# Kernel optimization log

Measured on AMD Instinct MI355X. Metric: run time of the kernel, lower is better.

## Reference

```python
import jax, jax.numpy as jnp
import numpy as np

# 4D conv over (L, P, W, H) decomposed as k shifted 3D convs over (P, W, H),
# with the L spatial dim folded into the batch. Faithful to convNd(num_dims=4),
# stride 1, 'same' padding (padding = (k-1)//2), no bias.

def conv4d(x, w):
    # x: [B, C, L, P, W, H]; w: [O, I, k, k, k, k]
    k = w.shape[2]
    p = (k - 1) // 2
    B, C, L, P, Wd, Hd = x.shape
    O = w.shape[0]
    xp = jnp.pad(x, ((0, 0), (0, 0), (p, p), (0, 0), (0, 0), (0, 0)))
    dn = ('NCDHW', 'OIDHW', 'NCDHW')
    out = jnp.zeros((B, O, L, P, Wd, Hd), x.dtype)
    for dl in range(k):  # k <= 3, static loop over kernel taps along L
        xs = xp[:, :, dl:dl + L]                                  # [B,C,L,P,W,H]
        xs = xs.transpose(0, 2, 1, 3, 4, 5).reshape(B * L, C, P, Wd, Hd)
        y = jax.lax.conv_general_dilated(xs, w[:, :, dl], (1, 1, 1),
                                         [(p, p)] * 3, dimension_numbers=dn)
        out = out + y.reshape(B, L, O, P, Wd, Hd).transpose(0, 2, 1, 3, 4, 5)
    return out


def inception4d(x, weights):
    # mean over parallel 4D convs with kernel sizes 1, 3, ... (2i+1)
    acc = conv4d(x, weights[0])
    for w in weights[1:]:
        acc = acc + conv4d(x, w)
    return acc / len(weights)


def setup_inputs() -> dict:
    key = jax.random.key(0)
    ks = jax.random.split(key, 5)
    B, T, W, H, C = 4, 48, 8, 8, 32
    d_model, d_ff = 32, 64
    x = jax.random.normal(ks[0], (B, T, W, H, C), dtype=jnp.float32)
    # Inception_Block4D weights: kernel sizes 1 and 3 (num_kernels=2), no bias
    w1_0 = jax.random.normal(ks[1], (d_ff, d_model, 1, 1, 1, 1), dtype=jnp.float32) * 0.1
    w1_1 = jax.random.normal(ks[2], (d_ff, d_model, 3, 3, 3, 3), dtype=jnp.float32) * 0.02
    w2_0 = jax.random.normal(ks[3], (d_model, d_ff, 1, 1, 1, 1), dtype=jnp.float32) * 0.1
    w2_1 = jax.random.normal(ks[4], (d_model, d_ff, 3, 3, 3, 3), dtype=jnp.float32) * 0.02
    return {"x": x, "w1_0": w1_0, "w1_1": w1_1, "w2_0": w2_0, "w2_1": w2_1}


def reference(x, w1_0, w1_1, w2_0, w2_1):
    B, T, W, H, C = x.shape
    periods = (2, 3, 4)                       # FFT_for_Period hardcoded output
    xf = jnp.ones((B, len(periods)), x.dtype) # hardcoded uniform weights
    real_len = T                              # seq_len + pred_len
    res = []
    for period in periods:
        if real_len % period != 0:
            length = (real_len // period + 1) * period
            out = jnp.concatenate([x, x[:, -(length - real_len):]], axis=1)
        else:
            length = real_len
            out = x
        # [B, L, P, W, H, C] -> [B, C, L, P, W, H]
        out = out.reshape(B, length // period, period, W, H, C).transpose(0, 5, 1, 2, 3, 4)
        h = inception4d(out, [w1_0, w1_1])
        h = jax.nn.gelu(h, approximate=False)  # torch nn.GELU default (exact)
        h = inception4d(h, [w2_0, w2_1])
        # [B, C, L, P, W, H] -> [B, (L P), W, H, C]
        h = h.transpose(0, 2, 3, 4, 5, 1).reshape(B, length, W, H, C)
        res.append(h[:, :real_len])
    res = jnp.stack(res, axis=1)              # [B, k, T, W, H, C]
    pw = jax.nn.softmax(xf, axis=1).reshape(B, len(periods), 1, 1, 1, 1)
    return jnp.sum(res * pw, axis=1) + x
```

## Files before the change

kernel.cpp:

```cpp
#include <hip/hip_runtime.h>
#include <math.h>


typedef __attribute__((ext_vector_type(8))) short bf16x8;
typedef __attribute__((ext_vector_type(4))) float f32x4;
typedef unsigned short u16;

#define XC 3200
#define HC2 7168
#define XSEG 617600
#define ZSEG_END 639104
#define W1OFF 639104
#define W2OFF 804992
#define H1OFF 970880
#define H1P 1383424
#define PREP_N 970880
#define OUT_Q 98304
#define PREP_TOT (PREP_N + OUT_Q)

#define WAITVM(N) asm volatile("s_waitcnt vmcnt(" #N ")" ::: "memory")
#define SBAR()    asm volatile("s_barrier" ::: "memory")

__device__ __forceinline__ u16 f2bf(float f) {
    unsigned u = __float_as_uint(f);
    unsigned r = u + 0x7fffu + ((u >> 16) & 1u);
    return (u16)(r >> 16);
}
__device__ __forceinline__ float gelu_exact(float v) {
    return 0.5f * v * (1.0f + erff(v * 0.7071067811865476f));
}

__device__ __forceinline__ void cp1k(const u16* g, u16* l, int lane) {
    __builtin_amdgcn_global_load_lds(
        (const __attribute__((address_space(1))) unsigned int*)(g + lane * 8),
        (__attribute__((address_space(3))) unsigned int*)(l + lane * 8),
        16, 0, 0);
}

__global__ __launch_bounds__(256) void prep(
    const float* __restrict__ x,
    const float* __restrict__ w1_0, const float* __restrict__ w1_1,
    const float* __restrict__ w2_0, const float* __restrict__ w2_1,
    u16* __restrict__ ws, float* __restrict__ out) {
    int i = blockIdx.x * 256 + threadIdx.x;
    if (i < XSEG) {
        int cellidx = i / XC; int inner = i - cellidx * XC;
        int cellpos = inner >> 5; int low = inner & 31;
        int sc = low >> 3, jj = low & 7;
        int c = ((sc ^ (cellpos & 3)) << 3) + jj;
        int wp = cellpos / 10, hp = cellpos - (cellpos / 10) * 10;
        float v = 0.f;
        if (cellidx < 192 && wp >= 1 && wp <= 8 && hp >= 1 && hp <= 8)
            v = x[(cellidx * 64 + (wp - 1) * 8 + (hp - 1)) * 32 + c];
        ws[i] = f2bf(v);
    } else if (i < ZSEG_END) {
        int j = i - XSEG;
        int per = j / 7168; int off = j - per * 7168;
        ws[H1OFF + per * H1P + 192 * 7168 + off] = 0;
    } else if (i < W2OFF) {
        int j = i - W1OFF;
        int tap = j >> 11; int r = j & 2047;
        int nh = r >> 10; int rr = r & 1023;
        int chunkh = rr >> 3, jj = rr & 7;
        int m = chunkh & 15, nq = (chunkh >> 4) & 1, quad = chunkh >> 5;
        int o = nh * 32 + nq * 16 + m, c = quad * 8 + jj;
        float v = 0.5f * w1_1[(o * 32 + c) * 81 + tap];
        if (tap == 40) v += 0.5f * w1_0[o * 32 + c];
        ws[i] = f2bf(v);
    } else if (i < PREP_N) {
        int j = i - W2OFF;
        int tap = j >> 11; int r = j & 2047;
        int kh = r >> 10; int rr = r & 1023;
        int chunkh = rr >> 3, jj = rr & 7;
        int m = chunkh & 15, nt = (chunkh >> 4) & 1, quad = chunkh >> 5;
        int o = nt * 16 + m, c = kh * 32 + quad * 8 + jj;
        float v = 0.5f * w2_1[(o * 64 + c) * 81 + tap];
        if (tap == 40) v += 0.5f * w2_0[o * 64 + c];
        ws[i] = f2bf(v);
    } else if (i < PREP_TOT) {
        int j = i - PREP_N;
        ((float4*)out)[j] = ((const float4*)x)[j];
    }
}

template<int P>
__device__ __forceinline__ void conv1_body(
    const u16* __restrict__ xs, const u16* __restrict__ w1b,
    u16* __restrict__ h1, int tpp, int bb, int nh,
    u16* __restrict__ s_a, u16* __restrict__ s_w) {
    constexpr int HB = (P == 2) ? 0 : (P == 3) ? H1P : 2 * H1P;
    constexpr int L = 48 / P;
    constexpr int EXT = P + 1;
    constexpr int NW = 6 + 2 * EXT;
    constexpr int ZS = NW;
    constexpr int NP = (NW + 1) * 7;

    int tid = threadIdx.x;
    int lane = tid & 63, wv = tid >> 6;
    int m = lane & 15, quad = lane >> 4;
    int ts = wv >> 1, mh = wv & 1;
    int t0 = tpp * 6, t = t0 + ts;
    int l = t / P, q = t - l * P;

    int sp[2];
#pragma unroll
    for (int mtl = 0; mtl < 2; ++mtl) {
        int pos = (mh * 2 + mtl) * 16 + m;
        sp[mtl] = (pos >> 3) * 10 + (pos & 7);
    }

    f32x4 acc[2][2];
#pragma unroll
    for (int mtl = 0; mtl < 2; ++mtl)
#pragma unroll
        for (int nq = 0; nq < 2; ++nq) acc[mtl][nq] = f32x4{0.f, 0.f, 0.f, 0.f};

    for (int p = wv; p < NP; p += 12) {
        int si = p / 7, pc = p - si * 7;
        int tt = t0 - EXT + si;
        int cell = (si == ZS) ? 192
                 : (((unsigned)tt < 48u) ? bb * 48 + tt : 192);
        cp1k(xs + cell * XC + pc * 512, s_a + si * 3584 + pc * 512, lane);
    }
    if (wv < 6) {
        cp1k(w1b + (0 * 3 + (wv >> 1)) * 2048 + nh * 1024 + (wv & 1) * 512,
             s_w + 0 * 3072 + wv * 512, lane);
        cp1k(w1b + (1 * 3 + (wv >> 1)) * 2048 + nh * 1024 + (wv & 1) * 512,
             s_w + 1 * 3072 + wv * 512, lane);
        WAITVM(1);
    } else {
        WAITVM(0);
    }
    SBAR();

#pragma unroll 1
    for (int cg = 0; cg < 27; ++cg) {
        if (wv < 6 && cg < 25)
            cp1k(w1b + ((cg + 2) * 3 + (wv >> 1)) * 2048 + nh * 1024 +
                     (wv & 1) * 512,
                 s_w + ((cg + 2) & 3) * 3072 + wv * 512, lane);
        if (cg < 25)       { WAITVM(2); }
        else if (cg == 25) { WAITVM(1); }
        else               { WAITVM(0); }
        SBAR();

        int g2 = cg / 3, dw = cg - g2 * 3;
        int dl = g2 / 3, dq = g2 - dl * 3;
        int lq = l + dl - 1, qq = q + dq - 1;
        bool valid = ((unsigned)lq < (unsigned)L) &&
                     ((unsigned)qq < (unsigned)P);
        int si = valid ? (ts + dl * P + dq) : ZS;
        const u16* ba = s_a + si * 3584;
        const u16* bw = s_w + (cg & 3) * 3072;
#pragma unroll
        for (int j = 0; j < 3; ++j) {
            const u16* tw = bw + j * 1024;
            bf16x8 wf0 = *(const bf16x8*)(tw + (((quad * 2 + 0) * 16 + m) << 3));
            bf16x8 wf1 = *(const bf16x8*)(tw + (((quad * 2 + 1) * 16 + m) << 3));
#pragma unroll
            for (int mtl = 0; mtl < 2; ++mtl) {
                int cellpos = sp[mtl] + dw * 10 + j;
                bf16x8 af = *(const bf16x8*)(ba + cellpos * 32 +
                                             ((quad ^ (cellpos & 3)) << 3));
                acc[mtl][0] = __builtin_amdgcn_mfma_f32_16x16x32_bf16(
                    af, wf0, acc[mtl][0], 0, 0, 0);
                acc[mtl][1] = __builtin_amdgcn_mfma_f32_16x16x32_bf16(
                    af, wf1, acc[mtl][1], 0, 0, 0);
            }
        }
    }

    u16* hh = h1 + HB + (bb * 48 + t) * HC2 + nh * 3584;
#pragma unroll
    for (int mtl = 0; mtl < 2; ++mtl)
#pragma unroll
        for (int r = 0; r < 4; ++r) {
            int pos = (mh * 2 + mtl) * 16 + quad * 4 + r;
            int cellpos = ((pos >> 3) + 1) * 10 + (pos & 7) + 1;
#pragma unroll
            for (int nq = 0; nq < 2; ++nq) {
                int ol = nq * 16 + m;
                hh[cellpos * 32 + (((ol >> 3) ^ (cellpos & 3)) << 3) + (ol & 7)] =
                    f2bf(gelu_exact(acc[mtl][nq][r]));
            }
        }
#pragma unroll
    for (int it = 0; it < 5; ++it) {
        int k = it * 768 + tid;
        if (k < 3456) {
            int tc = k / 576; int rr = k - tc * 576;
            int bp = rr >> 4, u = rr & 15;
            int cp;
            if (bp < 10) cp = bp;
            else if (bp < 20) cp = 90 + (bp - 10);
            else if (bp < 28) cp = (bp - 19) * 10;
            else cp = (bp - 27) * 10 + 9;
            unsigned int* h32 = (unsigned int*)(h1 + HB +
                (bb * 48 + t0 + tc) * HC2 + nh * 3584);
            h32[cp * 16 + u] = 0;
        }
    }
}

__global__ __launch_bounds__(768) void conv1_k(
    const u16* __restrict__ ws_x, const u16* __restrict__ ws_w1,
    u16* __restrict__ ws_h1) {
    __shared__ __align__(16) u16 s_a[17 * 3584];
    __shared__ __align__(16) u16 s_w[4 * 3072];
    int g = blockIdx.x;
    int jid = (g & 7) * 24 + (g >> 3);
    int per = jid / 64; int rem = jid - per * 64;
    int bb = rem / 16; int r2 = rem - bb * 16;
    int tpp = r2 >> 1, nh = r2 & 1;
    if (per == 0)      conv1_body<2>(ws_x, ws_w1, ws_h1, tpp, bb, nh, s_a, s_w);
    else if (per == 1) conv1_body<3>(ws_x, ws_w1, ws_h1, tpp, bb, nh, s_a, s_w);
    else               conv1_body<4>(ws_x, ws_w1, ws_h1, tpp, bb, nh, s_a, s_w);
}

template<int P>
__device__ __forceinline__ void conv2_body(
    const u16* __restrict__ h1, const u16* __restrict__ w2b,
    float* __restrict__ out, int tpp, int bb, int kh,
    u16* __restrict__ s_a, u16* __restrict__ s_w) {
    constexpr int HB = (P == 2) ? 0 : (P == 3) ? H1P : 2 * H1P;
    constexpr int L = 48 / P;
    constexpr int EXT = P + 1;
    constexpr int NW = 6 + 2 * EXT;
    constexpr int ZS = NW;
    constexpr int NP = (NW + 1) * 7;

    int tid = threadIdx.x;
    int lane = tid & 63, wv = tid >> 6;
    int m = lane & 15, quad = lane >> 4;
    int ts = wv >> 1, mh = wv & 1;
    int t0 = tpp * 6, t = t0 + ts;
    int l = t / P, q = t - l * P;
    const u16* hb = h1 + HB;

    int sp[2];
#pragma unroll
    for (int mtl = 0; mtl < 2; ++mtl) {
        int pos = (mh * 2 + mtl) * 16 + m;
        sp[mtl] = (pos >> 3) * 10 + (pos & 7);
    }

    f32x4 acc[2][2];
#pragma unroll
    for (int mtl = 0; mtl < 2; ++mtl)
#pragma unroll
        for (int nt = 0; nt < 2; ++nt) acc[mtl][nt] = f32x4{0.f, 0.f, 0.f, 0.f};

    for (int p = wv; p < NP; p += 12) {
        int si = p / 7, pc = p - si * 7;
        int tt = t0 - EXT + si;
        int cell = (si == ZS) ? 192
                 : (((unsigned)tt < 48u) ? bb * 48 + tt : 192);
        cp1k(hb + cell * HC2 + kh * 3584 + pc * 512,
             s_a + si * 3584 + pc * 512, lane);
    }
    if (wv < 6) {
        cp1k(w2b + (0 * 3 + (wv >> 1)) * 2048 + kh * 1024 + (wv & 1) * 512,
             s_w + 0 * 3072 + wv * 512, lane);
        cp1k(w2b + (1 * 3 + (wv >> 1)) * 2048 + kh * 1024 + (wv & 1) * 512,
             s_w + 1 * 3072 + wv * 512, lane);
        WAITVM(1);
    } else {
        WAITVM(0);
    }
    SBAR();

#pragma unroll 1
    for (int cg = 0; cg < 27; ++cg) {
        if (wv < 6 && cg < 25)
            cp1k(w2b + ((cg + 2) * 3 + (wv >> 1)) * 2048 + kh * 1024 +
                     (wv & 1) * 512,
                 s_w + ((cg + 2) & 3) * 3072 + wv * 512, lane);
        if (cg < 25)       { WAITVM(2); }
        else if (cg == 25) { WAITVM(1); }
        else               { WAITVM(0); }
        SBAR();

        int g2 = cg / 3, dw = cg - g2 * 3;
        int dl = g2 / 3, dq = g2 - dl * 3;
        int lq = l + dl - 1, qq = q + dq - 1;
        bool valid = ((unsigned)lq < (unsigned)L) &&
                     ((unsigned)qq < (unsigned)P);
        int si = valid ? (ts + dl * P + dq) : ZS;
        const u16* ba = s_a + si * 3584;
        const u16* bw = s_w + (cg & 3) * 3072;
#pragma unroll
        for (int j = 0; j < 3; ++j) {
            const u16* tw = bw + j * 1024;
            bf16x8 wf0 = *(const bf16x8*)(tw + (((quad * 2 + 0) * 16 + m) << 3));
            bf16x8 wf1 = *(const bf16x8*)(tw + (((quad * 2 + 1) * 16 + m) << 3));
#pragma unroll
            for (int mtl = 0; mtl < 2; ++mtl) {
                int cellpos = sp[mtl] + dw * 10 + j;
                bf16x8 af = *(const bf16x8*)(ba + cellpos * 32 +
                                             ((quad ^ (cellpos & 3)) << 3));
                acc[mtl][0] = __builtin_amdgcn_mfma_f32_16x16x32_bf16(
                    af, wf0, acc[mtl][0], 0, 0, 0);
                acc[mtl][1] = __builtin_amdgcn_mfma_f32_16x16x32_bf16(
                    af, wf1, acc[mtl][1], 0, 0, 0);
            }
        }
    }

    float* orow = out + (bb * 48 + t) * 2048;
    const float s = 1.0f / 3.0f;
#pragma unroll
    for (int mtl = 0; mtl < 2; ++mtl)
#pragma unroll
        for (int nt = 0; nt < 2; ++nt)
#pragma unroll
            for (int r = 0; r < 4; ++r) {
                int pos = (mh * 2 + mtl) * 16 + quad * 4 + r;
                atomicAdd(&orow[pos * 32 + nt * 16 + m], acc[mtl][nt][r] * s);
            }
}

__global__ __launch_bounds__(768) void conv2_k(
    const u16* __restrict__ ws_h1, const u16* __restrict__ ws_w2,
    float* __restrict__ out) {
    __shared__ __align__(16) u16 s_a[17 * 3584];
    __shared__ __align__(16) u16 s_w[4 * 3072];
    int g = blockIdx.x;
    int jid = (g & 7) * 24 + (g >> 3);
    int per = jid / 64; int rem = jid - per * 64;
    int bb = rem / 16; int r2 = rem - bb * 16;
    int tpp = r2 >> 1, kh = r2 & 1;
    if (per == 0)      conv2_body<2>(ws_h1, ws_w2, out, tpp, bb, kh, s_a, s_w);
    else if (per == 1) conv2_body<3>(ws_h1, ws_w2, out, tpp, bb, kh, s_a, s_w);
    else               conv2_body<4>(ws_h1, ws_w2, out, tpp, bb, kh, s_a, s_w);
}

extern "C" void kernel_launch(void* const* d_in, const int* in_sizes, int n_in,
                              void* d_out, int out_size, void* d_ws, size_t ws_size,
                              hipStream_t stream) {
    const float* x    = (const float*)d_in[0];
    const float* w1_0 = (const float*)d_in[1];
    const float* w1_1 = (const float*)d_in[2];
    const float* w2_0 = (const float*)d_in[3];
    const float* w2_1 = (const float*)d_in[4];
    float* out = (float*)d_out;

    u16* ws = (u16*)d_ws;
    u16* ws_x  = ws;
    u16* ws_w1 = ws + W1OFF;
    u16* ws_w2 = ws + W2OFF;
    u16* ws_h1 = ws + H1OFF;

    prep<<<(PREP_TOT + 255) / 256, 256, 0, stream>>>(
        x, w1_0, w1_1, w2_0, w2_1, ws, out);
    conv1_k<<<192, 768, 0, stream>>>(ws_x, ws_w1, ws_h1);
    conv2_k<<<192, 768, 0, stream>>>(ws_h1, ws_w2, out);
}
```

Baseline: 118.9 us.

## Stage weights per 9-tap group with double buffering, cutting barriers from 27 to 9

```diff
diff --git a/kernel.cpp b/kernel.cpp
--- a/kernel.cpp
+++ b/kernel.cpp
@@ -115,6 +115,17 @@
 #pragma unroll
         for (int nq = 0; nq < 2; ++nq) acc[mtl][nq] = f32x4{0.f, 0.f, 0.f, 0.f};
 
+    auto stageS = [&](int sg) {
+        const u16* src = w1b + nh * 1024;
+        u16* dst = s_w + (sg & 1) * 9216;
+#pragma unroll
+        for (int i = 0; i < 2; ++i) {
+            int k = wv * 2 + i; if (k >= 18) k = 17;
+            cp1k(src + (sg * 9 + (k >> 1)) * 2048 + (k & 1) * 512,
+                 dst + k * 512, lane);
+        }
+    };
+
     for (int p = wv; p < NP; p += 12) {
         int si = p / 7, pc = p - si * 7;
         int tt = t0 - EXT + si;
@@ -122,52 +133,41 @@
                  : (((unsigned)tt < 48u) ? bb * 48 + tt : 192);
         cp1k(xs + cell * XC + pc * 512, s_a + si * 3584 + pc * 512, lane);
     }
-    if (wv < 6) {
-        cp1k(w1b + (0 * 3 + (wv >> 1)) * 2048 + nh * 1024 + (wv & 1) * 512,
-             s_w + 0 * 3072 + wv * 512, lane);
-        cp1k(w1b + (1 * 3 + (wv >> 1)) * 2048 + nh * 1024 + (wv & 1) * 512,
-             s_w + 1 * 3072 + wv * 512, lane);
-        WAITVM(1);
-    } else {
-        WAITVM(0);
-    }
-    SBAR();
+    stageS(0);
+    WAITVM(0); SBAR();
 
 #pragma unroll 1
-    for (int cg = 0; cg < 27; ++cg) {
-        if (wv < 6 && cg < 25)
-            cp1k(w1b + ((cg + 2) * 3 + (wv >> 1)) * 2048 + nh * 1024 +
-                     (wv & 1) * 512,
-                 s_w + ((cg + 2) & 3) * 3072 + wv * 512, lane);
-        if (cg < 25)       { WAITVM(2); }
-        else if (cg == 25) { WAITVM(1); }
-        else               { WAITVM(0); }
-        SBAR();
-
-        int g2 = cg / 3, dw = cg - g2 * 3;
-        int dl = g2 / 3, dq = g2 - dl * 3;
+    for (int g = 0; g < 9; ++g) {
+        if (g < 8) stageS(g + 1);
+
+        int dl = g / 3, dq = g - dl * 3;
         int lq = l + dl - 1, qq = q + dq - 1;
         bool valid = ((unsigned)lq < (unsigned)L) &&
                      ((unsigned)qq < (unsigned)P);
         int si = valid ? (ts + dl * P + dq) : ZS;
         const u16* ba = s_a + si * 3584;
-        const u16* bw = s_w + (cg & 3) * 3072;
-#pragma unroll
-        for (int j = 0; j < 3; ++j) {
-            const u16* tw = bw + j * 1024;
-            bf16x8 wf0 = *(const bf16x8*)(tw + (((quad * 2 + 0) * 16 + m) << 3));
-            bf16x8 wf1 = *(const bf16x8*)(tw + (((quad * 2 + 1) * 16 + m) << 3));
-#pragma unroll
-            for (int mtl = 0; mtl < 2; ++mtl) {
-                int cellpos = sp[mtl] + dw * 10 + j;
-                bf16x8 af = *(const bf16x8*)(ba + cellpos * 32 +
-                                             ((quad ^ (cellpos & 3)) << 3));
-                acc[mtl][0] = __builtin_amdgcn_mfma_f32_16x16x32_bf16(
-                    af, wf0, acc[mtl][0], 0, 0, 0);
-                acc[mtl][1] = __builtin_amdgcn_mfma_f32_16x16x32_bf16(
-                    af, wf1, acc[mtl][1], 0, 0, 0);
+        const u16* bw = s_w + (g & 1) * 9216;
+#pragma unroll
+        for (int dw = 0; dw < 3; ++dw)
+#pragma unroll
+            for (int j = 0; j < 3; ++j) {
+                const u16* tw = bw + (dw * 3 + j) * 1024;
+                bf16x8 wf0 = *(const bf16x8*)(tw +
+                    (((quad * 2 + 0) * 16 + m) << 3));
+                bf16x8 wf1 = *(const bf16x8*)(tw +
+                    (((quad * 2 + 1) * 16 + m) << 3));
+#pragma unroll
+                for (int mtl = 0; mtl < 2; ++mtl) {
+                    int cellpos = sp[mtl] + dw * 10 + j;
+                    bf16x8 af = *(const bf16x8*)(ba + cellpos * 32 +
+                                                 ((quad ^ (cellpos & 3)) << 3));
+                    acc[mtl][0] = __builtin_amdgcn_mfma_f32_16x16x32_bf16(
+                        af, wf0, acc[mtl][0], 0, 0, 0);
+                    acc[mtl][1] = __builtin_amdgcn_mfma_f32_16x16x32_bf16(
+                        af, wf1, acc[mtl][1], 0, 0, 0);
+                }
             }
-        }
+        if (g < 8) { WAITVM(0); SBAR(); }
     }
 
     u16* hh = h1 + HB + (bb * 48 + t) * HC2 + nh * 3584;
@@ -206,7 +206,7 @@
     const u16* __restrict__ ws_x, const u16* __restrict__ ws_w1,
     u16* __restrict__ ws_h1) {
     __shared__ __align__(16) u16 s_a[17 * 3584];
-    __shared__ __align__(16) u16 s_w[4 * 3072];
+    __shared__ __align__(16) u16 s_w[2 * 9216];
     int g = blockIdx.x;
     int jid = (g & 7) * 24 + (g >> 3);
     int per = jid / 64; int rem = jid - per * 64;
@@ -250,6 +250,17 @@
 #pragma unroll
         for (int nt = 0; nt < 2; ++nt) acc[mtl][nt] = f32x4{0.f, 0.f, 0.f, 0.f};
 
+    auto stageS = [&](int sg) {
+        const u16* src = w2b + kh * 1024;
+        u16* dst = s_w + (sg & 1) * 9216;
+#pragma unroll
+        for (int i = 0; i < 2; ++i) {
+            int k = wv * 2 + i; if (k >= 18) k = 17;
+            cp1k(src + (sg * 9 + (k >> 1)) * 2048 + (k & 1) * 512,
+                 dst + k * 512, lane);
+        }
+    };
+
     for (int p = wv; p < NP; p += 12) {
         int si = p / 7, pc = p - si * 7;
         int tt = t0 - EXT + si;
@@ -258,52 +269,41 @@
         cp1k(hb + cell * HC2 + kh * 3584 + pc * 512,
              s_a + si * 3584 + pc * 512, lane);
     }
-    if (wv < 6) {
-        cp1k(w2b + (0 * 3 + (wv >> 1)) * 2048 + kh * 1024 + (wv & 1) * 512,
-             s_w + 0 * 3072 + wv * 512, lane);
-        cp1k(w2b + (1 * 3 + (wv >> 1)) * 2048 + kh * 1024 + (wv & 1) * 512,
-             s_w + 1 * 3072 + wv * 512, lane);
-        WAITVM(1);
-    } else {
-        WAITVM(0);
-    }
-    SBAR();
+    stageS(0);
+    WAITVM(0); SBAR();
 
 #pragma unroll 1
-    for (int cg = 0; cg < 27; ++cg) {
-        if (wv < 6 && cg < 25)
-            cp1k(w2b + ((cg + 2) * 3 + (wv >> 1)) * 2048 + kh * 1024 +
-                     (wv & 1) * 512,
-                 s_w + ((cg + 2) & 3) * 3072 + wv * 512, lane);
-        if (cg < 25)       { WAITVM(2); }
-        else if (cg == 25) { WAITVM(1); }
-        else               { WAITVM(0); }
-        SBAR();
-
-        int g2 = cg / 3, dw = cg - g2 * 3;
-        int dl = g2 / 3, dq = g2 - dl * 3;
+    for (int g = 0; g < 9; ++g) {
+        if (g < 8) stageS(g + 1);
+
+        int dl = g / 3, dq = g - dl * 3;
         int lq = l + dl - 1, qq = q + dq - 1;
         bool valid = ((unsigned)lq < (unsigned)L) &&
                      ((unsigned)qq < (unsigned)P);
         int si = valid ? (ts + dl * P + dq) : ZS;
         const u16* ba = s_a + si * 3584;
-        const u16* bw = s_w + (cg & 3) * 3072;
-#pragma unroll
-        for (int j = 0; j < 3; ++j) {
-            const u16* tw = bw + j * 1024;
-            bf16x8 wf0 = *(const bf16x8*)(tw + (((quad * 2 + 0) * 16 + m) << 3));
-            bf16x8 wf1 = *(const bf16x8*)(tw + (((quad * 2 + 1) * 16 + m) << 3));
-#pragma unroll
-            for (int mtl = 0; mtl < 2; ++mtl) {
-                int cellpos = sp[mtl] + dw * 10 + j;
-                bf16x8 af = *(const bf16x8*)(ba + cellpos * 32 +
-                                             ((quad ^ (cellpos & 3)) << 3));
-                acc[mtl][0] = __builtin_amdgcn_mfma_f32_16x16x32_bf16(
-                    af, wf0, acc[mtl][0], 0, 0, 0);
-                acc[mtl][1] = __builtin_amdgcn_mfma_f32_16x16x32_bf16(
-                    af, wf1, acc[mtl][1], 0, 0, 0);
+        const u16* bw = s_w + (g & 1) * 9216;
+#pragma unroll
+        for (int dw = 0; dw < 3; ++dw)
+#pragma unroll
+            for (int j = 0; j < 3; ++j) {
+                const u16* tw = bw + (dw * 3 + j) * 1024;
+                bf16x8 wf0 = *(const bf16x8*)(tw +
+                    (((quad * 2 + 0) * 16 + m) << 3));
+                bf16x8 wf1 = *(const bf16x8*)(tw +
+                    (((quad * 2 + 1) * 16 + m) << 3));
+#pragma unroll
+                for (int mtl = 0; mtl < 2; ++mtl) {
+                    int cellpos = sp[mtl] + dw * 10 + j;
+                    bf16x8 af = *(const bf16x8*)(ba + cellpos * 32 +
+                                                 ((quad ^ (cellpos & 3)) << 3));
+                    acc[mtl][0] = __builtin_amdgcn_mfma_f32_16x16x32_bf16(
+                        af, wf0, acc[mtl][0], 0, 0, 0);
+                    acc[mtl][1] = __builtin_amdgcn_mfma_f32_16x16x32_bf16(
+                        af, wf1, acc[mtl][1], 0, 0, 0);
+                }
             }
-        }
+        if (g < 8) { WAITVM(0); SBAR(); }
     }
 
     float* orow = out + (bb * 48 + t) * 2048;
@@ -323,7 +323,7 @@
     const u16* __restrict__ ws_h1, const u16* __restrict__ ws_w2,
     float* __restrict__ out) {
     __shared__ __align__(16) u16 s_a[17 * 3584];
-    __shared__ __align__(16) u16 s_w[4 * 3072];
+    __shared__ __align__(16) u16 s_w[2 * 9216];
     int g = blockIdx.x;
     int jid = (g & 7) * 24 + (g >> 3);
     int per = jid / 64; int rem = jid - per * 64;
```

Result: faster. 116.1 us (-2.3%).
